# Kernel tuning notes

Hardware: AMD Instinct MI355X
Metric: run time of the kernel (lower is better)

Reference implementation:

```python
import jax, jax.numpy as jnp
import numpy as np

H, KV, DH = 16, 4, 64  # num_heads, num_kv_heads, head_dim


def setup_inputs() -> dict:
    key = jax.random.key(0)
    k1, k2, k3, k4, k5 = jax.random.split(key, 5)
    B, L, D = 1, 4096, 1024
    s = 0.02
    return {
        "x": jax.random.normal(k1, (B, L, D), dtype=jnp.float32),
        "Wq": jax.random.normal(k2, (D, H * DH), dtype=jnp.float32) * s,
        "Wk": jax.random.normal(k3, (D, KV * DH), dtype=jnp.float32) * s,
        "Wv": jax.random.normal(k4, (D, KV * DH), dtype=jnp.float32) * s,
        "Wo": jax.random.normal(k5, (H * DH, D), dtype=jnp.float32) * s,
    }


def _rotate_half(t):
    t1, t2 = t[..., : DH // 2], t[..., DH // 2 :]
    return jnp.concatenate([-t2, t1], axis=-1)


def reference(x, Wq, Wk, Wv, Wo):
    B, L, D = x.shape
    G = H // KV  # query heads per kv head
    q = (x @ Wq).reshape(B, L, H, DH)
    k = (x @ Wk).reshape(B, L, KV, DH)
    v = (x @ Wv).reshape(B, L, KV, DH)

    # RoPE: inv_freq over even dims, angles duplicated across both halves
    inv_freq = 1.0 / (10000.0 ** (jnp.arange(0, DH, 2, dtype=jnp.float32) / DH))
    t = jnp.arange(L, dtype=jnp.float32)
    freqs = t[:, None] * inv_freq[None, :]                 # [L, DH/2]
    emb = jnp.concatenate([freqs, freqs], axis=-1)[None, :, None, :]  # [1,L,1,DH]
    cos, sin = jnp.cos(emb), jnp.sin(emb)
    q = q * cos + _rotate_half(q) * sin
    k = k * cos + _rotate_half(k) * sin

    # GQA: query head h attends with kv head h // G (repeat_interleave layout)
    qg = q.reshape(B, L, KV, G, DH)
    scale = DH ** -0.5
    attn = jnp.einsum("bqkgd,bskd->bkgqs", qg, k) * scale  # [B,KV,G,L,L]
    attn = jax.nn.softmax(attn, axis=-1)
    out = jnp.einsum("bkgqs,bskd->bqkgd", attn, v).reshape(B, L, H * DH)
    return out @ Wo
```

## Files before the change

### kernel.cpp

```cpp
#include <hip/hip_runtime.h>
#include <math.h>

#define L 4096
#define D 1024
#define H 16
#define KV 4
#define DH 64

typedef __attribute__((ext_vector_type(8))) short bf16x8;
typedef __attribute__((ext_vector_type(4))) float f32x4;
typedef __attribute__((ext_vector_type(16))) float f32x16;
typedef __attribute__((ext_vector_type(2))) unsigned int u32x2;

static __device__ __forceinline__ unsigned short f2bf(float f) {
    unsigned u = __float_as_uint(f);
    u = (u + 0x7FFF + ((u >> 16) & 1)) >> 16;
    return (unsigned short)u;
}

static __device__ __forceinline__ bf16x8 mk8(unsigned a, unsigned b, unsigned c, unsigned d) {
    union { unsigned u[4]; bf16x8 v; } x;
    x.u[0] = a; x.u[1] = b; x.u[2] = c; x.u[3] = d;
    return x.v;
}

#define EXP2F(x) __builtin_amdgcn_exp2f(x)
#define ZERO16 ((f32x16){0.f,0.f,0.f,0.f,0.f,0.f,0.f,0.f,0.f,0.f,0.f,0.f,0.f,0.f,0.f,0.f})

#define GLD16(src, dst) \
    __builtin_amdgcn_global_load_lds((__attribute__((address_space(1))) void*)(src), \
                                     (__attribute__((address_space(3))) void*)(dst), 16, 0, 0)

__global__ __launch_bounds__(256) void prep_kernel(
        const float* __restrict__ x,  const float* __restrict__ Wq,
        const float* __restrict__ Wk, const float* __restrict__ Wv,
        const float* __restrict__ Wo,
        unsigned short* __restrict__ xb, unsigned short* __restrict__ WqkvT,
        unsigned short* __restrict__ WoT) {
    const int b = blockIdx.x, tid = threadIdx.x;
    if (b < 4096) {
        int i = (b * 256 + tid) * 4;
        float4 v = *(const float4*)&x[i];
        ushort4 o;
        o.x = f2bf(v.x); o.y = f2bf(v.y); o.z = f2bf(v.z); o.w = f2bf(v.w);
        *(ushort4*)&xb[i] = o;
        return;
    }
    __shared__ float t[32][33];
    const float* src; unsigned short* dst; int N, n0, k0;
    if (b < 5120)      { int tq = b - 4096; src = Wq; dst = WqkvT;                     N = 1024; n0 = (tq & 31) * 32; k0 = (tq >> 5) * 32; }
    else if (b < 5376) { int tq = b - 5120; src = Wk; dst = WqkvT + (size_t)1024*1024; N = 256;  n0 = (tq & 7)  * 32; k0 = (tq >> 3) * 32; }
    else if (b < 5632) { int tq = b - 5376; src = Wv; dst = WqkvT + (size_t)1280*1024; N = 256;  n0 = (tq & 7)  * 32; k0 = (tq >> 3) * 32; }
    else               { int tq = b - 5632; src = Wo; dst = WoT;                       N = 1024; n0 = (tq & 31) * 32; k0 = (tq >> 5) * 32; }
    const int tx = tid & 31, ty = tid >> 5;
    #pragma unroll
    for (int j = 0; j < 4; ++j)
        t[ty + 8 * j][tx] = src[(size_t)(k0 + ty + 8 * j) * N + n0 + tx];
    __syncthreads();
    #pragma unroll
    for (int j = 0; j < 4; ++j)
        dst[(size_t)(n0 + ty + 8 * j) * 1024 + k0 + tx] = f2bf(t[tx][ty + 8 * j]);
}

__global__ __launch_bounds__(256) void gemm_bf16(const unsigned short* __restrict__ A,
                                                 const unsigned short* __restrict__ BT,
                                                 float* __restrict__ C,
                                                 int M, int N, int K) {
    __shared__ unsigned short As[64 * 32];
    __shared__ unsigned short Bs[128 * 32];

    const int tid  = threadIdx.x;
    const int w    = tid >> 6;
    const int lane = tid & 63;
    const int c    = lane & 15;
    const int quad = lane >> 4;
    const int wy = w >> 1, wx = w & 1;
    const int row0 = blockIdx.y * 64;
    const int col0 = blockIdx.x * 128;

    const int ld_row = lane >> 2;
    const int ld_col = (lane & 3) * 8;

    f32x4 acc[2][4];
    #pragma unroll
    for (int mt = 0; mt < 2; ++mt)
        #pragma unroll
        for (int nt = 0; nt < 4; ++nt)
            acc[mt][nt] = (f32x4){0.f, 0.f, 0.f, 0.f};

    for (int k0 = 0; k0 < K; k0 += 32) {
        __syncthreads();
        GLD16(&A [(size_t)(row0 + w * 16 + ld_row)      * K + k0 + ld_col], &As[w * 512]);
        GLD16(&BT[(size_t)(col0 + w * 16 + ld_row)      * K + k0 + ld_col], &Bs[w * 512]);
        GLD16(&BT[(size_t)(col0 + w * 16 + 64 + ld_row) * K + k0 + ld_col], &Bs[w * 512 + 2048]);
        __syncthreads();

        bf16x8 af[2], bfr[4];
        #pragma unroll
        for (int mt = 0; mt < 2; ++mt)
            af[mt] = *(const bf16x8*)&As[(wy * 32 + mt * 16 + c) * 32 + quad * 8];
        #pragma unroll
        for (int nt = 0; nt < 4; ++nt)
            bfr[nt] = *(const bf16x8*)&Bs[(wx * 64 + nt * 16 + c) * 32 + quad * 8];

        #pragma unroll
        for (int mt = 0; mt < 2; ++mt)
            #pragma unroll
            for (int nt = 0; nt < 4; ++nt)
                acc[mt][nt] = __builtin_amdgcn_mfma_f32_16x16x32_bf16(af[mt], bfr[nt], acc[mt][nt], 0, 0, 0);
    }

    #pragma unroll
    for (int mt = 0; mt < 2; ++mt)
        #pragma unroll
        for (int nt = 0; nt < 4; ++nt)
            #pragma unroll
            for (int r = 0; r < 4; ++r)
                C[(size_t)(row0 + wy * 32 + mt * 16 + quad * 4 + r) * N
                  + col0 + wx * 64 + nt * 16 + c] = acc[mt][nt][r];
}

__global__ __launch_bounds__(256) void gemm_qkv_rope(
        const unsigned short* __restrict__ A,
        const unsigned short* __restrict__ BT,
        unsigned short* __restrict__ qb,
        unsigned short* __restrict__ kbuf,
        unsigned short* __restrict__ vbuf) {
    __shared__ unsigned short As[64 * 32];
    __shared__ unsigned short Bs[128 * 32];

    const int tid  = threadIdx.x;
    const int w    = tid >> 6;
    const int lane = tid & 63;
    const int c    = lane & 15;
    const int quad = lane >> 4;
    const int wy = w >> 1, wx = w & 1;
    const int row0 = blockIdx.y * 64;
    const int col0 = blockIdx.x * 128;

    const int ld_row = lane >> 2;
    const int ld_col = (lane & 3) * 8;

    f32x4 acc[2][4];
    #pragma unroll
    for (int mt = 0; mt < 2; ++mt)
        #pragma unroll
        for (int nt = 0; nt < 4; ++nt)
            acc[mt][nt] = (f32x4){0.f, 0.f, 0.f, 0.f};

    for (int k0 = 0; k0 < 1024; k0 += 32) {
        __syncthreads();
        GLD16(&A [(size_t)(row0 + w * 16 + ld_row)      * 1024 + k0 + ld_col], &As[w * 512]);
        GLD16(&BT[(size_t)(col0 + w * 16 + ld_row)      * 1024 + k0 + ld_col], &Bs[w * 512]);
        GLD16(&BT[(size_t)(col0 + w * 16 + 64 + ld_row) * 1024 + k0 + ld_col], &Bs[w * 512 + 2048]);
        __syncthreads();

        bf16x8 af[2], bfr[4];
        #pragma unroll
        for (int mt = 0; mt < 2; ++mt)
            af[mt] = *(const bf16x8*)&As[(wy * 32 + mt * 16 + c) * 32 + quad * 8];
        #pragma unroll
        for (int nt = 0; nt < 4; ++nt)
            bfr[nt] = *(const bf16x8*)&Bs[(wx * 64 + nt * 16 + c) * 32 + quad * 8];

        #pragma unroll
        for (int mt = 0; mt < 2; ++mt)
            #pragma unroll
            for (int nt = 0; nt < 4; ++nt)
                acc[mt][nt] = __builtin_amdgcn_mfma_f32_16x16x32_bf16(af[mt], bfr[nt], acc[mt][nt], 0, 0, 0);
    }

    const int colb = col0 + wx * 64;
    if (colb < 1280) {
        unsigned short* dst; int hh, hstride; float scale;
        if (colb < 1024) { dst = qb;   hh = colb >> 6;          hstride = H;  scale = 0.18033688011112042f; }
        else             { dst = kbuf; hh = (colb - 1024) >> 6; hstride = KV; scale = 1.0f; }
        #pragma unroll
        for (int nt = 0; nt < 2; ++nt) {
            int d = nt * 16 + c;
            float invf = EXP2F((float)d * -0.4152410118609203f);
            #pragma unroll
            for (int mt = 0; mt < 2; ++mt)
                #pragma unroll
                for (int r = 0; r < 4; ++r) {
                    int l = row0 + wy * 32 + mt * 16 + quad * 4 + r;
                    float ang = (float)l * invf;
                    float sn = __sinf(ang), cs = __cosf(ang);
                    float x1 = acc[mt][nt][r], x2 = acc[mt][nt + 2][r];
                    dst[((size_t)l * hstride + hh) * DH + d]      = f2bf((x1 * cs - x2 * sn) * scale);
                    dst[((size_t)l * hstride + hh) * DH + d + 32] = f2bf((x2 * cs + x1 * sn) * scale);
                }
        }
    } else {
        int vh = (colb - 1280) >> 6;
        #pragma unroll
        for (int mt = 0; mt < 2; ++mt)
            #pragma unroll
            for (int nt = 0; nt < 4; ++nt)
                #pragma unroll
                for (int r = 0; r < 4; ++r) {
                    int l = row0 + wy * 32 + mt * 16 + quad * 4 + r;
                    vbuf[((size_t)l * KV + vh) * DH + nt * 16 + c] = f2bf(acc[mt][nt][r]);
                }
    }
}

__global__ __attribute__((amdgpu_flat_work_group_size(512, 512), amdgpu_waves_per_eu(2)))
void attn_mfma_kernel(
        const unsigned short* __restrict__ qb,
        const unsigned short* __restrict__ kb,
        const unsigned short* __restrict__ vb,
        unsigned short* __restrict__ ob) {
    __shared__ __align__(16) unsigned short Vt[2][2][64][64];
    __shared__ __align__(16) float Ep[4][64][64];
    __shared__ __align__(16) float Rs[8][2][32];

    const int tid  = threadIdx.x;
    const int w    = tid >> 6;
    const int lane = tid & 63;
    const int c32  = lane & 31;
    const int hi   = lane >> 5;
    const int g    = w >> 2;
    const int kv = blockIdx.y;
    const int h  = kv * 4 + (w & 3);
    const int q0 = blockIdx.x * 64;
    const int s_base = g * 2048;

    bf16x8 qf[2][4];
    {
        const unsigned short* qbase = qb + ((size_t)(q0 + c32) * H + h) * DH + hi * 8;
        #pragma unroll
        for (int qt = 0; qt < 2; ++qt)
            #pragma unroll
            for (int kd = 0; kd < 4; ++kd)
                qf[qt][kd] = *(const bf16x8*)&qbase[qt * 32 * H * DH + kd * 16];
    }

    f32x16 oacc[2][2];
    #pragma unroll
    for (int qt = 0; qt < 2; ++qt)
        #pragma unroll
        for (int dt = 0; dt < 2; ++dt)
            oacc[qt][dt] = ZERO16;
    float rsum[2] = {0.f, 0.f};

    const int tid8 = tid & 255;
    const int sp = tid8 & 31, dc = tid8 >> 5;

    const unsigned short* kbase = kb + ((size_t)(s_base + c32) * KV + kv) * DH + hi * 8;
    const unsigned short* vbase = vb + ((size_t)(s_base + 2 * sp) * KV + kv) * DH + dc * 8;
    unsigned short* VtW = &Vt[g][0][0][0];

    int4 vreg0 = *(const int4*)&vbase[0];
    int4 vreg1 = *(const int4*)&vbase[KV * DH];
    bf16x8 kf[2][4];
    #pragma unroll
    for (int a = 0; a < 2; ++a)
        #pragma unroll
        for (int kd = 0; kd < 4; ++kd)
            kf[a][kd] = *(const bf16x8*)&kbase[a * 32 * KV * DH + kd * 16];

    for (int it = 0; it < 32; ++it) {
        const int bufo = (it & 1) * (64 * 64);

        {
            const unsigned* pa = (const unsigned*)&vreg0;
            const unsigned* pb = (const unsigned*)&vreg1;
            #pragma unroll
            for (int t = 0; t < 4; ++t) {
                unsigned lo = __builtin_amdgcn_perm(pb[t], pa[t], 0x05040100u);
                unsigned hv = __builtin_amdgcn_perm(pb[t], pa[t], 0x07060302u);
                int dl = dc * 8 + 2 * t, dh2 = dl + 1;
                *(unsigned*)&VtW[bufo + dl  * 64 + (((sp >> 2) ^ (dl  & 7)) << 3) + 2 * (sp & 3)] = lo;
                *(unsigned*)&VtW[bufo + dh2 * 64 + (((sp >> 2) ^ (dh2 & 7)) << 3) + 2 * (sp & 3)] = hv;
            }
        }
        __syncthreads();

        const int itn = (it + 1) & 31;
        vreg0 = *(const int4*)&vbase[(size_t)itn * 64 * KV * DH];
        vreg1 = *(const int4*)&vbase[(size_t)itn * 64 * KV * DH + KV * DH];

        #pragma unroll
        for (int kt2 = 0; kt2 < 2; ++kt2) {
            bf16x8 pf[2][2];
            #pragma unroll
            for (int qt = 0; qt < 2; ++qt) {
                f32x16 s = ZERO16;
                #pragma unroll
                for (int kd = 0; kd < 4; ++kd)
                    s = __builtin_amdgcn_mfma_f32_32x32x16_bf16(kf[kt2][kd], qf[qt][kd], s, 0, 0, 0);
                float p[16];
                #pragma unroll
                for (int r = 0; r < 16; ++r)
                    p[r] = __uint_as_float(__float_as_uint(EXP2F(s[r])) & 0xFFFF0000u);
                float t0 = (p[0] + p[1]) + (p[2] + p[3]);
                float t1 = (p[4] + p[5]) + (p[6] + p[7]);
                float t2 = (p[8] + p[9]) + (p[10] + p[11]);
                float t3 = (p[12] + p[13]) + (p[14] + p[15]);
                rsum[qt] += (t0 + t1) + (t2 + t3);
                unsigned u[8];
                #pragma unroll
                for (int i = 0; i < 8; ++i)
                    u[i] = __builtin_amdgcn_perm(__float_as_uint(p[2 * i + 1]),
                                                 __float_as_uint(p[2 * i]), 0x07060302u);
                #pragma unroll
                for (int f = 0; f < 2; ++f) {
                    u32x2 e0 = __builtin_amdgcn_permlane32_swap(u[4 * f + 0], u[4 * f + 2], false, false);
                    u32x2 e1 = __builtin_amdgcn_permlane32_swap(u[4 * f + 1], u[4 * f + 3], false, false);
                    pf[qt][f] = mk8(e0.x, e1.x, e0.y, e1.y);
                }
            }
            if (kt2 == 1) {
                #pragma unroll
                for (int a = 0; a < 2; ++a)
                    #pragma unroll
                    for (int kd = 0; kd < 4; ++kd)
                        kf[a][kd] = *(const bf16x8*)&kbase[((size_t)itn * 64 + a * 32) * KV * DH + kd * 16];
            }
            __builtin_amdgcn_s_setprio(1);
            #pragma unroll
            for (int dt = 0; dt < 2; ++dt)
                #pragma unroll
                for (int f = 0; f < 2; ++f) {
                    bf16x8 vf = *(const bf16x8*)&VtW[bufo + (dt * 32 + c32) * 64
                                    + ((((kt2 * 4 + f * 2 + hi) ^ (c32 & 7)) << 3))];
                    #pragma unroll
                    for (int qt = 0; qt < 2; ++qt)
                        oacc[qt][dt] = __builtin_amdgcn_mfma_f32_32x32x16_bf16(pf[qt][f], vf, oacc[qt][dt], 0, 0, 0);
                }
            __builtin_amdgcn_s_setprio(0);
        }
    }

    #pragma unroll
    for (int qt = 0; qt < 2; ++qt) {
        u32x2 e = __builtin_amdgcn_permlane32_swap(__float_as_uint(rsum[qt]),
                                                   __float_as_uint(rsum[qt]), false, false);
        float tot = __uint_as_float(e.x) + __uint_as_float(e.y);
        Rs[w][qt][c32] = tot;
    }
    if (g == 1) {
        #pragma unroll
        for (int qt = 0; qt < 2; ++qt)
            #pragma unroll
            for (int dt = 0; dt < 2; ++dt) {
                const int d = dt * 32 + c32;
                #pragma unroll
                for (int rr = 0; rr < 4; ++rr) {
                    const int gq = (qt * 8 + 2 * rr + hi) ^ (d & 15);
                    f32x4 val = {oacc[qt][dt][rr * 4 + 0], oacc[qt][dt][rr * 4 + 1],
                                 oacc[qt][dt][rr * 4 + 2], oacc[qt][dt][rr * 4 + 3]};
                    *(f32x4*)&Ep[w - 4][d][gq * 4] = val;
                }
            }
    }
    __syncthreads();
    if (g == 0) {
        #pragma unroll
        for (int qt = 0; qt < 2; ++qt)
            #pragma unroll
            for (int dt = 0; dt < 2; ++dt) {
                const int d = dt * 32 + c32;
                #pragma unroll
                for (int rr = 0; rr < 4; ++rr) {
                    const int gq = (qt * 8 + 2 * rr + hi) ^ (d & 15);
                    f32x4 val = *(const f32x4*)&Ep[w][d][gq * 4];
                    oacc[qt][dt][rr * 4 + 0] += val[0];
                    oacc[qt][dt][rr * 4 + 1] += val[1];
                    oacc[qt][dt][rr * 4 + 2] += val[2];
                    oacc[qt][dt][rr * 4 + 3] += val[3];
                }
            }
        #pragma unroll
        for (int qt = 0; qt < 2; ++qt)
            #pragma unroll
            for (int rr = 0; rr < 4; ++rr) {
                f32x4 ra = *(const f32x4*)&Rs[w][qt][8 * rr + 4 * hi];
                f32x4 rb = *(const f32x4*)&Rs[w + 4][qt][8 * rr + 4 * hi];
                #pragma unroll
                for (int i = 0; i < 4; ++i) {
                    float inv = 1.0f / (ra[i] + rb[i]);
                    int row = q0 + qt * 32 + 8 * rr + 4 * hi + i;
                    #pragma unroll
                    for (int dt = 0; dt < 2; ++dt)
                        ob[(size_t)row * (H * DH) + h * DH + dt * 32 + c32] =
                            f2bf(oacc[qt][dt][rr * 4 + i] * inv);
                }
            }
    }
}

extern "C" void kernel_launch(void* const* d_in, const int* in_sizes, int n_in,
                              void* d_out, int out_size, void* d_ws, size_t ws_size,
                              hipStream_t stream) {
    const float* x  = (const float*)d_in[0];
    const float* Wq = (const float*)d_in[1];
    const float* Wk = (const float*)d_in[2];
    const float* Wv = (const float*)d_in[3];
    const float* Wo = (const float*)d_in[4];
    float* out = (float*)d_out;

    char* ws = (char*)d_ws;
    unsigned short* xb    = (unsigned short*)ws;
    unsigned short* ob    = xb;
    unsigned short* qb    = (unsigned short*)(ws + 8388608);
    unsigned short* kb    = (unsigned short*)(ws + 16777216);
    unsigned short* vb    = (unsigned short*)(ws + 18874368);
    unsigned short* WqkvT = (unsigned short*)(ws + 20971520);
    unsigned short* WoT   = (unsigned short*)(ws + 24117248);

    dim3 blk(256);

    prep_kernel<<<6656, blk, 0, stream>>>(x, Wq, Wk, Wv, Wo, xb, WqkvT, WoT);

    gemm_qkv_rope<<<dim3(12, 64), blk, 0, stream>>>(xb, WqkvT, qb, kb, vb);

    attn_mfma_kernel<<<dim3(L / 64, KV), dim3(512), 0, stream>>>(qb, kb, vb, ob);

    gemm_bf16<<<dim3(D / 128, L / 64), blk, 0, stream>>>(ob, WoT, out, L, D, D);
}
```

Before: 205.5 us.

## Store V transposed from QKV GEMM and stream it per-wave via direct-to-LDS loads

The QKV GEMM now writes V transposed ([kv*DH, L]), so the attention kernel no longer loads V into registers, permutes it and transposes it into LDS. Each wave streams its own swizzled V tile straight into a private double-buffered LDS region with direct global-to-LDS loads, synchronised by a vmcnt wait instead of a block-wide __syncthreads per iteration. The cost is 8x more LDS for V (the epilogue buffer now aliases it) and redundant V loads per wave, which may lower occupancy.

```diff
diff --git a/kernel.cpp b/kernel.cpp
--- a/kernel.cpp
+++ b/kernel.cpp
@@ -125,7 +125,7 @@
         const unsigned short* __restrict__ BT,
         unsigned short* __restrict__ qb,
         unsigned short* __restrict__ kbuf,
-        unsigned short* __restrict__ vbuf) {
+        unsigned short* __restrict__ vbT) {
     __shared__ unsigned short As[64 * 32];
     __shared__ unsigned short Bs[128 * 32];
 
@@ -194,14 +194,15 @@
     } else {
         int vh = (colb - 1280) >> 6;
         #pragma unroll
-        for (int mt = 0; mt < 2; ++mt)
-            #pragma unroll
-            for (int nt = 0; nt < 4; ++nt)
-                #pragma unroll
-                for (int r = 0; r < 4; ++r) {
-                    int l = row0 + wy * 32 + mt * 16 + quad * 4 + r;
-                    vbuf[((size_t)l * KV + vh) * DH + nt * 16 + c] = f2bf(acc[mt][nt][r]);
-                }
+        for (int nt = 0; nt < 4; ++nt)
+            #pragma unroll
+            for (int mt = 0; mt < 2; ++mt) {
+                int l = row0 + wy * 32 + mt * 16 + quad * 4;
+                ushort4 o;
+                o.x = f2bf(acc[mt][nt][0]); o.y = f2bf(acc[mt][nt][1]);
+                o.z = f2bf(acc[mt][nt][2]); o.w = f2bf(acc[mt][nt][3]);
+                *(ushort4*)&vbT[(size_t)(vh * DH + nt * 16 + c) * L + l] = o;
+            }
     }
 }
 
@@ -209,10 +210,9 @@
 void attn_mfma_kernel(
         const unsigned short* __restrict__ qb,
         const unsigned short* __restrict__ kb,
-        const unsigned short* __restrict__ vb,
+        const unsigned short* __restrict__ vbT,
         unsigned short* __restrict__ ob) {
-    __shared__ __align__(16) unsigned short Vt[2][2][64][64];
-    __shared__ __align__(16) float Ep[4][64][64];
+    __shared__ __align__(16) unsigned short Vt[8][2][64][64];
     __shared__ __align__(16) float Rs[8][2][32];
 
     const int tid  = threadIdx.x;
@@ -226,6 +226,11 @@
     const int q0 = blockIdx.x * 64;
     const int s_base = g * 2048;
 
+    const unsigned short* vbase = vbT + ((size_t)kv * DH) * L + s_base;
+    const int lr = lane >> 3;
+    const int laneoff = lr * L + (((lane & 7) ^ lr) << 3);
+    unsigned short* VtW = &Vt[w][0][0][0];
+
     bf16x8 qf[2][4];
     {
         const unsigned short* qbase = qb + ((size_t)(q0 + c32) * H + h) * DH + hi * 8;
@@ -244,42 +249,32 @@
             oacc[qt][dt] = ZERO16;
     float rsum[2] = {0.f, 0.f};
 
-    const int tid8 = tid & 255;
-    const int sp = tid8 & 31, dc = tid8 >> 5;
-
     const unsigned short* kbase = kb + ((size_t)(s_base + c32) * KV + kv) * DH + hi * 8;
-    const unsigned short* vbase = vb + ((size_t)(s_base + 2 * sp) * KV + kv) * DH + dc * 8;
-    unsigned short* VtW = &Vt[g][0][0][0];
-
-    int4 vreg0 = *(const int4*)&vbase[0];
-    int4 vreg1 = *(const int4*)&vbase[KV * DH];
+
     bf16x8 kf[2][4];
     #pragma unroll
     for (int a = 0; a < 2; ++a)
         #pragma unroll
         for (int kd = 0; kd < 4; ++kd)
             kf[a][kd] = *(const bf16x8*)&kbase[a * 32 * KV * DH + kd * 16];
+    {
+        const unsigned short* vs = vbase + laneoff;
+        #pragma unroll
+        for (int s = 0; s < 8; ++s)
+            GLD16(vs + s * (8 * L), VtW + s * 512);
+    }
 
     for (int it = 0; it < 32; ++it) {
-        const int bufo = (it & 1) * (64 * 64);
-
-        {
-            const unsigned* pa = (const unsigned*)&vreg0;
-            const unsigned* pb = (const unsigned*)&vreg1;
-            #pragma unroll
-            for (int t = 0; t < 4; ++t) {
-                unsigned lo = __builtin_amdgcn_perm(pb[t], pa[t], 0x05040100u);
-                unsigned hv = __builtin_amdgcn_perm(pb[t], pa[t], 0x07060302u);
-                int dl = dc * 8 + 2 * t, dh2 = dl + 1;
-                *(unsigned*)&VtW[bufo + dl  * 64 + (((sp >> 2) ^ (dl  & 7)) << 3) + 2 * (sp & 3)] = lo;
-                *(unsigned*)&VtW[bufo + dh2 * 64 + (((sp >> 2) ^ (dh2 & 7)) << 3) + 2 * (sp & 3)] = hv;
-            }
+        const int bufo = (it & 1) * 4096;
+        const int itn = (it + 1) & 31;
+
+        if (it != 31) {
+            const unsigned short* vs = vbase + itn * 64 + laneoff;
+            #pragma unroll
+            for (int s = 0; s < 8; ++s)
+                GLD16(vs + s * (8 * L), VtW + (bufo ^ 4096) + s * 512);
         }
-        __syncthreads();
-
-        const int itn = (it + 1) & 31;
-        vreg0 = *(const int4*)&vbase[(size_t)itn * 64 * KV * DH];
-        vreg1 = *(const int4*)&vbase[(size_t)itn * 64 * KV * DH + KV * DH];
+        asm volatile("s_waitcnt vmcnt(8)" ::: "memory");
 
         #pragma unroll
         for (int kt2 = 0; kt2 < 2; ++kt2) {
@@ -340,6 +335,8 @@
         float tot = __uint_as_float(e.x) + __uint_as_float(e.y);
         Rs[w][qt][c32] = tot;
     }
+    __syncthreads();
+    float (*Ep)[64][64] = (float (*)[64][64])&Vt[0][0][0][0];
     if (g == 1) {
         #pragma unroll
         for (int qt = 0; qt < 2; ++qt)
@@ -406,7 +403,7 @@
     unsigned short* ob    = xb;
     unsigned short* qb    = (unsigned short*)(ws + 8388608);
     unsigned short* kb    = (unsigned short*)(ws + 16777216);
-    unsigned short* vb    = (unsigned short*)(ws + 18874368);
+    unsigned short* vbT   = (unsigned short*)(ws + 18874368);
     unsigned short* WqkvT = (unsigned short*)(ws + 20971520);
     unsigned short* WoT   = (unsigned short*)(ws + 24117248);
 
@@ -414,9 +411,9 @@
 
     prep_kernel<<<6656, blk, 0, stream>>>(x, Wq, Wk, Wv, Wo, xb, WqkvT, WoT);
 
-    gemm_qkv_rope<<<dim3(12, 64), blk, 0, stream>>>(xb, WqkvT, qb, kb, vb);
-
-    attn_mfma_kernel<<<dim3(L / 64, KV), dim3(512), 0, stream>>>(qb, kb, vb, ob);
+    gemm_qkv_rope<<<dim3(12, 64), blk, 0, stream>>>(xb, WqkvT, qb, kb, vbT);
+
+    attn_mfma_kernel<<<dim3(L / 64, KV), dim3(512), 0, stream>>>(qb, kb, vbT, ob);
 
     gemm_bf16<<<dim3(D / 128, L / 64), blk, 0, stream>>>(ob, WoT, out, L, D, D);
 }
```

New measurement: 218.6 us. +6.4%, slower.
